# Performance work log

Hardware: AMD Instinct MI355X
Metric: run time of the kernel (lower is better)

The kernel has to match this reference:

```python
import jax, jax.numpy as jnp
import numpy as np

B, S, D, H = 2, 2048, 1024, 16
DK = D // H


def setup_inputs() -> dict:
    key = jax.random.key(0)
    ks = jax.random.split(key, 11)
    s = 1.0 / np.sqrt(D)
    inp = {
        "q": jax.random.normal(ks[0], (B, S, D), jnp.float32),
        "k": jax.random.normal(ks[1], (B, S, D), jnp.float32),
        "v": jax.random.normal(ks[2], (B, S, D), jnp.float32),
        # causal (lower-triangular) decoder mask, broadcast over batch & heads
        "mask": jnp.tril(jnp.ones((S, S), jnp.int32))[None, None, :, :],
        "Wq": jax.random.normal(ks[3], (D, D), jnp.float32) * s,
        "bq": jax.random.normal(ks[4], (D,), jnp.float32) * s,
        "Wk": jax.random.normal(ks[5], (D, D), jnp.float32) * s,
        "bk": jax.random.normal(ks[6], (D,), jnp.float32) * s,
        "Wv": jax.random.normal(ks[7], (D, D), jnp.float32) * s,
        "bv": jax.random.normal(ks[8], (D,), jnp.float32) * s,
        "Wo": jax.random.normal(ks[9], (D, D), jnp.float32) * s,
        "bo": jax.random.normal(ks[10], (D,), jnp.float32) * s,
    }
    return inp


def reference(q, k, v, mask, Wq, bq, Wk, bk, Wv, bv, Wo, bo):
    # projections (nn.Linear: x @ W.T + b)
    def proj(x, W, b):
        return (x @ W.T + b).reshape(B, S, H, DK).transpose(0, 2, 1, 3)  # [B,H,S,DK]

    Q = proj(q, Wq, bq)
    K = proj(k, Wk, bk)
    V = proj(v, Wv, bv)

    scores = jnp.einsum("bhsd,bhtd->bhst", Q, K) / jnp.sqrt(jnp.float32(DK))
    scores = jnp.where(mask == 0, jnp.float32(-1e9), scores)
    attn = jax.nn.softmax(scores, axis=-1)  # dropout=0.0 -> identity
    ctx = jnp.einsum("bhst,bhtd->bhsd", attn, V)
    ctx = ctx.transpose(0, 2, 1, 3).reshape(B, S, D)
    return ctx @ Wo.T + bo
```

## Files before the change

### kernel.cpp

```cpp
#include <hip/hip_runtime.h>

typedef __bf16 bf16;
typedef __bf16 bf16x8 __attribute__((ext_vector_type(8)));
typedef float floatx4 __attribute__((ext_vector_type(4)));

#define NB 2
#define NS 2048
#define ND 1024
#define NH 16
#define NDK 64
#define NM (NB * NS)

__device__ __forceinline__ void async_cp16(const void* g, void* l) {
  __builtin_amdgcn_global_load_lds(
      (const __attribute__((address_space(1))) void*)g,
      (__attribute__((address_space(3))) void*)l, 16, 0, 0);
}

__device__ __forceinline__ bf16x8 cvt8(const float* p) {
  float4 lo = *(const float4*)p, hi = *(const float4*)(p + 4);
  bf16x8 o;
  o[0] = (bf16)lo.x; o[1] = (bf16)lo.y; o[2] = (bf16)lo.z; o[3] = (bf16)lo.w;
  o[4] = (bf16)hi.x; o[5] = (bf16)hi.y; o[6] = (bf16)hi.z; o[7] = (bf16)hi.w;
  return o;
}

__device__ __forceinline__ void wg_barrier_lds() {
  __asm__ __volatile__("s_waitcnt lgkmcnt(0)" ::: "memory");
  __builtin_amdgcn_s_barrier();
}

struct CvtArgs {
  const float* src[8];
  bf16* dst[8];
  int nblk[8];
  int nseg;
};

__global__ __launch_bounds__(256) void cvt_kernel(CvtArgs a) {
  int b = blockIdx.x, seg = 0;
  while (seg < a.nseg - 1 && b >= a.nblk[seg]) { b -= a.nblk[seg]; ++seg; }
  const size_t idx = ((size_t)b * 256 + threadIdx.x) * 8;
  *(bf16x8*)(a.dst[seg] + idx) = cvt8(a.src[seg] + idx);
}

template <int TM, typename TA, typename TC>
__global__ __launch_bounds__(256) void gemm_dma(
    const TA* __restrict__ A0, const TA* __restrict__ A1, const TA* __restrict__ A2,
    const bf16* __restrict__ W0, const bf16* __restrict__ W1, const bf16* __restrict__ W2,
    const float* __restrict__ bias0, const float* __restrict__ bias1, const float* __restrict__ bias2,
    TC* __restrict__ C0, TC* __restrict__ C1, TC* __restrict__ C2)
{
  const int z = blockIdx.z;
  const TA* A = (z == 0) ? A0 : (z == 1) ? A1 : A2;
  const bf16* W = (z == 0) ? W0 : (z == 1) ? W1 : W2;
  const float* bias = (z == 0) ? bias0 : (z == 1) ? bias1 : bias2;
  TC* C = (z == 0) ? C0 : (z == 1) ? C1 : C2;

  __shared__ bf16 At[TM * 32];
  __shared__ bf16 Bt[128 * 32];

  const int tid = threadIdx.x;
  const int wave = tid >> 6, lane = tid & 63;
  const int q4 = lane >> 4, l15 = lane & 15;
  const int m0 = blockIdx.y * TM, n0 = blockIdx.x * 128;
  constexpr int WM = TM / 2;
  constexpr int MI = WM / 16;
  const int wm = (wave >> 1) * WM, wn = (wave & 1) * 64;

  floatx4 acc[MI][4] = {};

  const bf16* Wg = W + (size_t)(n0 + (lane >> 2)) * ND + (lane & 3) * 8;
  const bf16* Ag = nullptr;
  const float* Af = nullptr;
  const int srow = tid >> 2, sk = (tid & 3) * 8;
  if constexpr (sizeof(TA) == 2)
    Ag = (const bf16*)A + (size_t)(m0 + (lane >> 2)) * ND + (lane & 3) * 8;
  else
    Af = (const float*)A + (size_t)(m0 + srow) * ND + sk;

  for (int k0 = 0; k0 < ND; k0 += 32) {
    bf16x8 a0, a1;
    if constexpr (sizeof(TA) == 4) {
      a0 = cvt8(Af + k0);
      if constexpr (TM == 128) a1 = cvt8(Af + (size_t)64 * ND + k0);
    }
    __syncthreads();
#pragma unroll
    for (int c2 = 0; c2 < 2; ++c2) {
      const int c = wave * 2 + c2;
      async_cp16(Wg + (size_t)c * 16 * ND + k0, &Bt[c * 16 * 32]);
    }
    if constexpr (sizeof(TA) == 2) {
#pragma unroll
      for (int c2 = 0; c2 < TM / 64; ++c2) {
        const int c = wave * (TM / 64) + c2;
        async_cp16(Ag + (size_t)c * 16 * ND + k0, &At[c * 16 * 32]);
      }
    } else {
      *(bf16x8*)&At[srow * 32 + sk] = a0;
      if constexpr (TM == 128) *(bf16x8*)&At[(srow + 64) * 32 + sk] = a1;
    }
    __syncthreads();

    bf16x8 af[MI], bfr[4];
#pragma unroll
    for (int i = 0; i < MI; ++i)
      af[i] = *(const bf16x8*)&At[(wm + i * 16 + l15) * 32 + q4 * 8];
#pragma unroll
    for (int j = 0; j < 4; ++j)
      bfr[j] = *(const bf16x8*)&Bt[(wn + j * 16 + l15) * 32 + q4 * 8];
#pragma unroll
    for (int i = 0; i < MI; ++i)
#pragma unroll
      for (int j = 0; j < 4; ++j)
        acc[i][j] = __builtin_amdgcn_mfma_f32_16x16x32_bf16(af[i], bfr[j], acc[i][j], 0, 0, 0);
  }

#pragma unroll
  for (int j = 0; j < 4; ++j) {
    const int col = n0 + wn + j * 16 + l15;
    const float bv = bias[col];
#pragma unroll
    for (int i = 0; i < MI; ++i) {
      const int rowb = m0 + wm + i * 16 + q4 * 4;
#pragma unroll
      for (int r = 0; r < 4; ++r)
        C[(size_t)(rowb + r) * ND + col] = (TC)(acc[i][j][r] + bv);
    }
  }
}

#define NEGBIG (-1e30f)
#define LDV 72

__global__ __launch_bounds__(256) void attn_kernel(
    const bf16* __restrict__ Q, const bf16* __restrict__ K,
    const bf16* __restrict__ V, bf16* __restrict__ O)
{
  __shared__ bf16 vt[2][64 * LDV];
  __shared__ bf16 pbuf[4][16 * LDV];

  const int bx = blockIdx.x;
  const int h = blockIdx.y, b = blockIdx.z;
  const int tid = threadIdx.x, wave = tid >> 6, lane = tid & 63;
  const int q4 = lane >> 4, l15 = lane & 15;
  const int sl = lane;
  const int dbase = wave * 8;

  const bf16* kp = K + ((size_t)(b * NS) + l15) * ND + h * NDK + q4 * 8;
  const bf16* vp = V + ((size_t)(b * NS) + sl) * ND + h * NDK + dbase;

  bf16x8 qf[2];
  floatx4 oacc[4];
  float psum[4];
  bf16x8 kA[8], vA[2], kB[8], vB[2];

  auto ldK = [&](int j, bf16x8 (&kk)[8]) {
    const bf16* p = kp + (size_t)j * (64 * ND);
#pragma unroll
    for (int nf = 0; nf < 4; ++nf)
#pragma unroll
      for (int t = 0; t < 2; ++t)
        kk[nf * 2 + t] = *(const bf16x8*)(p + (size_t)nf * 16 * ND + t * 32);
  };
  auto ldV = [&](int j, bf16x8 (&vv)[2]) {
    const bf16* p = vp + (size_t)j * (64 * ND);
    vv[0] = *(const bf16x8*)(p);
    vv[1] = *(const bf16x8*)(p + 32);
  };

  auto body = [&](int j, int iq, bf16x8 (&kc)[8], bf16x8 (&vc)[2],
                  bf16x8 (&kn)[8], bf16x8 (&vn)[2]) {
    const int cur = j & 1;
#pragma unroll
    for (int it = 0; it < 2; ++it)
#pragma unroll
      for (int e = 0; e < 8; ++e)
        vt[cur][(dbase + it * 32 + e) * LDV + sl] = vc[it][e];

    if (j < iq) ldV(j + 1, vn);

    floatx4 sf[4];
    __builtin_amdgcn_s_setprio(1);
#pragma unroll
    for (int nf = 0; nf < 4; ++nf) {
      floatx4 s = {0.f, 0.f, 0.f, 0.f};
      s = __builtin_amdgcn_mfma_f32_16x16x32_bf16(qf[0], kc[nf * 2 + 0], s, 0, 0, 0);
      s = __builtin_amdgcn_mfma_f32_16x16x32_bf16(qf[1], kc[nf * 2 + 1], s, 0, 0, 0);
      sf[nf] = s;
    }
    __builtin_amdgcn_s_setprio(0);

    if (j < iq) ldK(j + 1, kn);

    wg_barrier_lds();

    if (j == iq) {
#pragma unroll
      for (int nf = 0; nf < 4; ++nf) {
        const int kc2 = nf * 16 + l15;
#pragma unroll
        for (int r = 0; r < 4; ++r)
          if (kc2 > wave * 16 + q4 * 4 + r) sf[nf][r] = NEGBIG;
      }
    }

#pragma unroll
    for (int nf = 0; nf < 4; ++nf)
#pragma unroll
      for (int r = 0; r < 4; ++r) {
        const float pv = exp2f(sf[nf][r]);
        psum[r] += pv;
        pbuf[wave][(q4 * 4 + r) * LDV + nf * 16 + l15] = (bf16)pv;
      }
    __asm__ __volatile__("s_waitcnt lgkmcnt(0)" ::: "memory");

    __builtin_amdgcn_s_setprio(1);
#pragma unroll
    for (int nf = 0; nf < 4; ++nf)
#pragma unroll
      for (int t = 0; t < 2; ++t) {
        bf16x8 pa = *(const bf16x8*)&pbuf[wave][l15 * LDV + t * 32 + q4 * 8];
        bf16x8 vb = *(const bf16x8*)&vt[cur][(nf * 16 + l15) * LDV + t * 32 + q4 * 8];
        oacc[nf] = __builtin_amdgcn_mfma_f32_16x16x32_bf16(pa, vb, oacc[nf], 0, 0, 0);
      }
    __builtin_amdgcn_s_setprio(0);
  };

  for (int ph = 0; ph < 2; ++ph) {
    const int iq = ph ? (31 - bx) : bx;
    __syncthreads();

    const size_t qrow0 = (size_t)(b * NS + iq * 64 + wave * 16 + l15);
#pragma unroll
    for (int t = 0; t < 2; ++t) {
      bf16x8 tmp = *(const bf16x8*)(Q + qrow0 * ND + h * NDK + t * 32 + q4 * 8);
#pragma unroll
      for (int e = 0; e < 8; ++e) qf[t][e] = (bf16)((float)tmp[e] * 0.180336880f);
    }

#pragma unroll
    for (int nf = 0; nf < 4; ++nf) oacc[nf] = floatx4{0.f, 0.f, 0.f, 0.f};
#pragma unroll
    for (int r = 0; r < 4; ++r) psum[r] = 0.f;

    ldK(0, kA); ldV(0, vA);
    for (int j = 0; j <= iq; ++j) {
      if ((j & 1) == 0) body(j, iq, kA, vA, kB, vB);
      else              body(j, iq, kB, vB, kA, vA);
    }

#pragma unroll
    for (int r = 0; r < 4; ++r)
#pragma unroll
      for (int off = 1; off < 16; off <<= 1) psum[r] += __shfl_xor(psum[r], off, 16);

#pragma unroll
    for (int nf = 0; nf < 4; ++nf)
#pragma unroll
      for (int r = 0; r < 4; ++r) {
        const int qrow = iq * 64 + wave * 16 + q4 * 4 + r;
        O[(size_t)(b * NS + qrow) * ND + h * NDK + nf * 16 + l15] =
            (bf16)(oacc[nf][r] / psum[r]);
      }
  }
}

extern "C" void kernel_launch(void* const* d_in, const int* in_sizes, int n_in,
                              void* d_out, int out_size, void* d_ws, size_t ws_size,
                              hipStream_t stream) {
  const float* q  = (const float*)d_in[0];
  const float* k  = (const float*)d_in[1];
  const float* v  = (const float*)d_in[2];
  const float* Wq = (const float*)d_in[4];
  const float* bq = (const float*)d_in[5];
  const float* Wk = (const float*)d_in[6];
  const float* bk = (const float*)d_in[7];
  const float* Wv = (const float*)d_in[8];
  const float* bv = (const float*)d_in[9];
  const float* Wo = (const float*)d_in[10];
  const float* bo = (const float*)d_in[11];
  float* out = (float*)d_out;
  char* w = (char*)d_ws;

  const dim3 attn_grid(NS / 128, NH, NB);

  if (ws_size >= (size_t)56 << 20) {
    bf16* xq = (bf16*)(w);
    bf16* xk = (bf16*)(w + ((size_t)8 << 20));
    bf16* xv = (bf16*)(w + ((size_t)16 << 20));
    bf16* wq = (bf16*)(w + ((size_t)24 << 20));
    bf16* wk = (bf16*)(w + ((size_t)26 << 20));
    bf16* wv = (bf16*)(w + ((size_t)28 << 20));
    bf16* wo = (bf16*)(w + ((size_t)30 << 20));
    bf16* Qb = (bf16*)(w + ((size_t)32 << 20));
    bf16* Kb = (bf16*)(w + ((size_t)40 << 20));
    bf16* Vb = (bf16*)(w + ((size_t)48 << 20));
    bf16* Ob = xq;

    CvtArgs ca{};
    const int b4 = (int)((size_t)NM * ND / 2048);
    const int b1 = (int)((size_t)ND * ND / 2048);
    ca.src[0] = q;  ca.dst[0] = xq; ca.nblk[0] = b4;
    ca.src[1] = k;  ca.dst[1] = xk; ca.nblk[1] = b4;
    ca.src[2] = v;  ca.dst[2] = xv; ca.nblk[2] = b4;
    ca.src[3] = Wq; ca.dst[3] = wq; ca.nblk[3] = b1;
    ca.src[4] = Wk; ca.dst[4] = wk; ca.nblk[4] = b1;
    ca.src[5] = Wv; ca.dst[5] = wv; ca.nblk[5] = b1;
    ca.src[6] = Wo; ca.dst[6] = wo; ca.nblk[6] = b1;
    ca.nseg = 7;
    cvt_kernel<<<3 * b4 + 4 * b1, 256, 0, stream>>>(ca);

    gemm_dma<128, bf16, bf16><<<dim3(8, 32, 3), 256, 0, stream>>>(
        xq, xk, xv, wq, wk, wv, bq, bk, bv, Qb, Kb, Vb);
    attn_kernel<<<attn_grid, 256, 0, stream>>>(Qb, Kb, Vb, Ob);
    gemm_dma<64, bf16, float><<<dim3(8, 64, 1), 256, 0, stream>>>(
        Ob, Ob, Ob, wo, wo, wo, bo, bo, bo, out, out, out);
  } else if (ws_size >= (size_t)40 << 20) {
    bf16* wq = (bf16*)(w);
    bf16* wk = (bf16*)(w + ((size_t)2 << 20));
    bf16* wv = (bf16*)(w + ((size_t)4 << 20));
    bf16* wo = (bf16*)(w + ((size_t)6 << 20));
    bf16* Qb = (bf16*)(w + ((size_t)8 << 20));
    bf16* Kb = (bf16*)(w + ((size_t)16 << 20));
    bf16* Vb = (bf16*)(w + ((size_t)24 << 20));
    bf16* Ob = (bf16*)(w + ((size_t)32 << 20));

    CvtArgs ca{};
    const int b1 = (int)((size_t)ND * ND / 2048);
    ca.src[0] = Wq; ca.dst[0] = wq; ca.nblk[0] = b1;
    ca.src[1] = Wk; ca.dst[1] = wk; ca.nblk[1] = b1;
    ca.src[2] = Wv; ca.dst[2] = wv; ca.nblk[2] = b1;
    ca.src[3] = Wo; ca.dst[3] = wo; ca.nblk[3] = b1;
    ca.nseg = 4;
    cvt_kernel<<<4 * b1, 256, 0, stream>>>(ca);

    gemm_dma<128, float, bf16><<<dim3(8, 32, 3), 256, 0, stream>>>(
        q, k, v, wq, wk, wv, bq, bk, bv, Qb, Kb, Vb);
    attn_kernel<<<attn_grid, 256, 0, stream>>>(Qb, Kb, Vb, Ob);
    gemm_dma<64, bf16, float><<<dim3(8, 64, 1), 256, 0, stream>>>(
        Ob, Ob, Ob, wo, wo, wo, bo, bo, bo, out, out, out);
  }
}
```

Before: 272.5 us.

## Stage V tiles via async LDS DMA and read with hardware transpose loads

V tiles are now copied from global memory straight into LDS with global_load_lds, laid out to suit ds_read_b64_tr_b16. This replaces the register round-trip and the element-by-element transposing LDS stores. The P·V MFMA operands then come from hardware transposed LDS reads issued before the softmax exponentials, and the next K/V prefetch moves after the barrier. It aims to cut LDS store traffic and VALU work in the attention inner loop. In exchange it relies on vmcnt ordering, not an explicit wait, to make the DMA'd V visible, and on a fairly intricate address swizzle being correct.

```diff
diff --git a/kernel.cpp b/kernel.cpp
--- a/kernel.cpp
+++ b/kernel.cpp
@@ -1,6 +1,7 @@
 #include <hip/hip_runtime.h>
 
 typedef __bf16 bf16;
+typedef __bf16 bf16x4 __attribute__((ext_vector_type(4)));
 typedef __bf16 bf16x8 __attribute__((ext_vector_type(8)));
 typedef float floatx4 __attribute__((ext_vector_type(4)));
 
@@ -28,6 +29,13 @@
 __device__ __forceinline__ void wg_barrier_lds() {
   __asm__ __volatile__("s_waitcnt lgkmcnt(0)" ::: "memory");
   __builtin_amdgcn_s_barrier();
+}
+
+__device__ __forceinline__ void tr2(const void* p, bf16x4& lo, bf16x4& hi) {
+  asm volatile("ds_read_b64_tr_b16 %0, %2\n\t"
+               "ds_read_b64_tr_b16 %1, %2 offset:512"
+               : "=&v"(lo), "=&v"(hi)
+               : "v"((const __attribute__((address_space(3))) void*)p));
 }
 
 struct CvtArgs {
@@ -132,29 +140,37 @@
 }
 
 #define NEGBIG (-1e30f)
-#define LDV 72
+#define LDP 72
 
 __global__ __launch_bounds__(256) void attn_kernel(
     const bf16* __restrict__ Q, const bf16* __restrict__ K,
     const bf16* __restrict__ V, bf16* __restrict__ O)
 {
-  __shared__ bf16 vt[2][64 * LDV];
-  __shared__ bf16 pbuf[4][16 * LDV];
+  __shared__ bf16 vt[2][4096];
+  __shared__ bf16 pbuf[4][16 * LDP];
 
   const int bx = blockIdx.x;
   const int h = blockIdx.y, b = blockIdx.z;
   const int tid = threadIdx.x, wave = tid >> 6, lane = tid & 63;
   const int q4 = lane >> 4, l15 = lane & 15;
-  const int sl = lane;
-  const int dbase = wave * 8;
 
   const bf16* kp = K + ((size_t)(b * NS) + l15) * ND + h * NDK + q4 * 8;
-  const bf16* vp = V + ((size_t)(b * NS) + sl) * ND + h * NDK + dbase;
+
+  const int sg0 = wave * 8 + (lane >> 3);
+  const int sg1 = 32 + sg0;
+  const int vs0 = ((sg0 >> 2) << 2) + ((lane & 7) >> 1);
+  const int vs1 = ((sg1 >> 2) << 2) + ((lane & 7) >> 1);
+  const int vd0 = (sg0 & 3) * 16 + (lane & 1) * 8;
+  const int vd1 = (sg1 & 3) * 16 + (lane & 1) * 8;
+  const bf16* vp0 = V + ((size_t)(b * NS) + vs0) * ND + h * NDK + vd0;
+  const bf16* vp1 = V + ((size_t)(b * NS) + vs1) * ND + h * NDK + vd1;
+
+  const int trb = (lane >> 4) * 512 + l15 * 4;
 
   bf16x8 qf[2];
   floatx4 oacc[4];
   float psum[4];
-  bf16x8 kA[8], vA[2], kB[8], vB[2];
+  bf16x8 kA[8], kB[8];
 
   auto ldK = [&](int j, bf16x8 (&kk)[8]) {
     const bf16* p = kp + (size_t)j * (64 * ND);
@@ -164,22 +180,14 @@
       for (int t = 0; t < 2; ++t)
         kk[nf * 2 + t] = *(const bf16x8*)(p + (size_t)nf * 16 * ND + t * 32);
   };
-  auto ldV = [&](int j, bf16x8 (&vv)[2]) {
-    const bf16* p = vp + (size_t)j * (64 * ND);
-    vv[0] = *(const bf16x8*)(p);
-    vv[1] = *(const bf16x8*)(p + 32);
+  auto stageV = [&](int j, int buf) {
+    const size_t off = (size_t)j * (64 * ND);
+    async_cp16(vp0 + off, &vt[buf][wave * 512]);
+    async_cp16(vp1 + off, &vt[buf][2048 + wave * 512]);
   };
 
-  auto body = [&](int j, int iq, bf16x8 (&kc)[8], bf16x8 (&vc)[2],
-                  bf16x8 (&kn)[8], bf16x8 (&vn)[2]) {
+  auto body = [&](int j, int iq, bf16x8 (&kc)[8], bf16x8 (&kn)[8]) {
     const int cur = j & 1;
-#pragma unroll
-    for (int it = 0; it < 2; ++it)
-#pragma unroll
-      for (int e = 0; e < 8; ++e)
-        vt[cur][(dbase + it * 32 + e) * LDV + sl] = vc[it][e];
-
-    if (j < iq) ldV(j + 1, vn);
 
     floatx4 sf[4];
     __builtin_amdgcn_s_setprio(1);
@@ -192,9 +200,13 @@
     }
     __builtin_amdgcn_s_setprio(0);
 
-    if (j < iq) ldK(j + 1, kn);
-
     wg_barrier_lds();
+
+    if (j < iq) {
+      stageV(j + 1, cur ^ 1);
+      asm volatile("" ::: "memory");
+      ldK(j + 1, kn);
+    }
 
     if (j == iq) {
 #pragma unroll
@@ -206,25 +218,36 @@
       }
     }
 
+    bf16x4 vlo[4][2], vhi[4][2];
+#pragma unroll
+    for (int nf = 0; nf < 4; ++nf)
+#pragma unroll
+      for (int t = 0; t < 2; ++t)
+        tr2(&vt[cur][t * 2048 + nf * 64 + trb], vlo[nf][t], vhi[nf][t]);
+
 #pragma unroll
     for (int nf = 0; nf < 4; ++nf)
 #pragma unroll
       for (int r = 0; r < 4; ++r) {
         const float pv = exp2f(sf[nf][r]);
         psum[r] += pv;
-        pbuf[wave][(q4 * 4 + r) * LDV + nf * 16 + l15] = (bf16)pv;
+        pbuf[wave][(q4 * 4 + r) * LDP + nf * 16 + l15] = (bf16)pv;
       }
-    __asm__ __volatile__("s_waitcnt lgkmcnt(0)" ::: "memory");
+
+    asm volatile("s_waitcnt lgkmcnt(0)" ::: "memory");
+    __builtin_amdgcn_sched_barrier(0);
+
+    bf16x8 pa0 = *(const bf16x8*)&pbuf[wave][l15 * LDP + q4 * 8];
+    bf16x8 pa1 = *(const bf16x8*)&pbuf[wave][l15 * LDP + 32 + q4 * 8];
 
     __builtin_amdgcn_s_setprio(1);
 #pragma unroll
-    for (int nf = 0; nf < 4; ++nf)
-#pragma unroll
-      for (int t = 0; t < 2; ++t) {
-        bf16x8 pa = *(const bf16x8*)&pbuf[wave][l15 * LDV + t * 32 + q4 * 8];
-        bf16x8 vb = *(const bf16x8*)&vt[cur][(nf * 16 + l15) * LDV + t * 32 + q4 * 8];
-        oacc[nf] = __builtin_amdgcn_mfma_f32_16x16x32_bf16(pa, vb, oacc[nf], 0, 0, 0);
-      }
+    for (int nf = 0; nf < 4; ++nf) {
+      bf16x8 vb0 = __builtin_shufflevector(vlo[nf][0], vhi[nf][0], 0, 1, 2, 3, 4, 5, 6, 7);
+      bf16x8 vb1 = __builtin_shufflevector(vlo[nf][1], vhi[nf][1], 0, 1, 2, 3, 4, 5, 6, 7);
+      oacc[nf] = __builtin_amdgcn_mfma_f32_16x16x32_bf16(pa0, vb0, oacc[nf], 0, 0, 0);
+      oacc[nf] = __builtin_amdgcn_mfma_f32_16x16x32_bf16(pa1, vb1, oacc[nf], 0, 0, 0);
+    }
     __builtin_amdgcn_s_setprio(0);
   };
 
@@ -245,10 +268,12 @@
 #pragma unroll
     for (int r = 0; r < 4; ++r) psum[r] = 0.f;
 
-    ldK(0, kA); ldV(0, vA);
+    stageV(0, 0);
+    asm volatile("" ::: "memory");
+    ldK(0, kA);
     for (int j = 0; j <= iq; ++j) {
-      if ((j & 1) == 0) body(j, iq, kA, vA, kB, vB);
-      else              body(j, iq, kB, vB, kA, vA);
+      if ((j & 1) == 0) body(j, iq, kA, kB);
+      else              body(j, iq, kB, kA);
     }
 
 #pragma unroll
```

Result: faster. 260.8 us (-4.3%).
